# Kernel tuning notes

Hardware: AMD Instinct MI355X
Metric: run time of the kernel (lower is better)

The kernel has to match this reference:

```python
import jax, jax.numpy as jnp
import numpy as np

K = 7          # involution kernel size
PAD = 3        # (K-1)//2
G = 4          # groups = out_channels // group_channels
GC = 16        # group_channels
EPS = 1e-5     # BatchNorm eps


def _bn(x, g, b, m, v):
    # eval-mode BatchNorm2d over channel dim of NCHW
    scale = g / jnp.sqrt(v + EPS)
    return x * scale[:, None, None] + (b - m * scale)[:, None, None]


def _conv1x1(x, w, b=None):
    y = jnp.einsum('bchw,oc->bohw', x, w)
    if b is not None:
        y = y + b[:, None, None]
    return y


def _gelu(x):
    return jax.nn.gelu(x, approximate=False)  # torch nn.GELU default (erf)


def _involution(x, wr, gr, br, mr, vr, ws, bs):
    # kernel-generation branch: 1x1 reduce -> BN -> ReLU -> 1x1 span
    r = jax.nn.relu(_bn(_conv1x1(x, wr), gr, br, mr, vr))
    w = _conv1x1(r, ws, bs)                       # [B, G*K*K, H, W]
    B, _, H, W = w.shape
    w = w.reshape(B, G, K * K, H, W)
    # unfold x into KxK patches (channel-major then row-major kernel pos, matching nn.Unfold)
    xp = jnp.pad(x, ((0, 0), (0, 0), (PAD, PAD), (PAD, PAD)))
    patches = jnp.stack([xp[:, :, i:i + H, j:j + W]
                         for i in range(K) for j in range(K)], axis=2)  # [B, C, KK, H, W]
    patches = patches.reshape(B, G, GC, K * K, H, W)
    out = jnp.einsum('bgkhw,bgckhw->bgchw', w, patches)  # per-pixel dynamic kernel apply
    return out.reshape(B, G * GC, H, W)


def setup_inputs() -> dict:
    key = jax.random.key(0)
    ks = jax.random.split(key, 24)
    B, Cin, Cout, H, W = 4, 32, 64, 128, 128
    red = Cout // 4
    n = lambda k, s, sc: jax.random.normal(k, s, jnp.float32) * sc
    u = lambda k, s: jax.random.uniform(k, s, jnp.float32, 0.5, 1.5)
    inp = {
        'x': n(ks[0], (B, Cin, H, W), 1.0),
        'w1': n(ks[1], (Cout, Cin), 0.15),
        # involution: reduce conv + BN, span conv
        'wr': n(ks[2], (red, Cout), 0.12), 'gr': u(ks[3], (red,)), 'br': n(ks[4], (red,), 0.05),
        'mr': n(ks[5], (red,), 0.05), 'vr': u(ks[6], (red,)),
        'ws': n(ks[7], (K * K * G, red), 0.1), 'bs': n(ks[8], (K * K * G,), 0.02),
        # BN after involution
        'g1': u(ks[9], (Cout,)), 'b1': n(ks[10], (Cout,), 0.05),
        'm1': n(ks[11], (Cout,), 0.05), 'v1': u(ks[12], (Cout,)),
        # convblock2
        'w2': n(ks[13], (Cout, Cout), 0.12),
        'g2': u(ks[14], (Cout,)), 'b2': n(ks[15], (Cout,), 0.05),
        'm2': n(ks[16], (Cout,), 0.05), 'v2': u(ks[17], (Cout,)),
        # mapping (residual projection) conv has bias=True by default
        'wm': n(ks[18], (Cout, Cin), 0.15), 'bmap': n(ks[19], (Cout,), 0.02),
        'gm': u(ks[20], (Cout,)), 'betam': n(ks[21], (Cout,), 0.05),
        'mm': n(ks[22], (Cout,), 0.05), 'vm': u(ks[23], (Cout,)),
    }
    return inp


def reference(x, w1, wr, gr, br, mr, vr, ws, bs, g1, b1, m1, v1,
              w2, g2, b2, m2, v2, wm, bmap, gm, betam, mm, vm):
    x1 = _gelu(_conv1x1(x, w1))                                  # convblock
    x1 = _gelu(_bn(_involution(x1, wr, gr, br, mr, vr, ws, bs),
                   g1, b1, m1, v1))                              # involution + BN + GELU
    x1 = _bn(_conv1x1(x1, w2), g2, b2, m2, v2)                   # convblock2
    skip = _bn(_conv1x1(x, wm, bmap), gm, betam, mm, vm)         # mapping (Cin != Cout)
    return _gelu(x1 + skip)
```

## Files before the change

### kernel.cpp

```cpp
#include <hip/hip_runtime.h>
#include <hip/hip_bf16.h>
#include <math.h>

#define HW    16384
#define Bsz   4
#define CIN   32
#define COUT  64
#define RED   16
#define KKN   49
#define GG    4
#define PW    134
#define PPLANE (PW*PW)
#define N16PAD 574592

typedef __hip_bfloat16 bf16;
typedef __attribute__((ext_vector_type(8))) short bf16x8;
typedef __attribute__((ext_vector_type(4))) float f32x4;

__device__ __forceinline__ float gelu_f(float x) {
    return 0.5f * x * (1.0f + erff(x * 0.70710678118654752f));
}
__device__ __forceinline__ void unpack_bf2(unsigned u, float& lo, float& hi) {
    lo = __uint_as_float(u << 16);
    hi = __uint_as_float(u & 0xffff0000u);
}
__device__ __forceinline__ unsigned pack_bf2(float lo, float hi) {
    unsigned a = __float_as_uint(lo), b = __float_as_uint(hi);
    a += 0x7fff + ((a >> 16) & 1);
    b += 0x7fff + ((b >> 16) & 1);
    return (a >> 16) | (b & 0xffff0000u);
}
__device__ __forceinline__ unsigned short bf16r(float v) {
    unsigned a = __float_as_uint(v);
    a += 0x7fff + ((a >> 16) & 1);
    return (unsigned short)(a >> 16);
}

#define OFF_RBUF  9437184
#define OFF_X2B   13631488
#define OFF_PAR   22020096
#define OFF_XBF   22085632
#define PW1T 0
#define PWRT 2048
#define PRSH 3072
#define PSHC (PRSH+16)
#define PSMV (PSHC+64)
#define PSC1 (PSMV+64)
#define PSH1 (PSC1+64)
#define PCAT_F 12288

__global__ __launch_bounds__(256) void k0_init(
    const float* __restrict__ w1, const float* __restrict__ wr,
    const float* __restrict__ gr, const float* __restrict__ br,
    const float* __restrict__ mr, const float* __restrict__ vr,
    const float* __restrict__ g1, const float* __restrict__ b1,
    const float* __restrict__ m1, const float* __restrict__ v1,
    const float* __restrict__ w2, const float* __restrict__ g2,
    const float* __restrict__ b2, const float* __restrict__ m2,
    const float* __restrict__ v2,
    const float* __restrict__ wm, const float* __restrict__ bmap,
    const float* __restrict__ gm, const float* __restrict__ betam,
    const float* __restrict__ mm, const float* __restrict__ vm,
    float* __restrict__ par, uint4* __restrict__ x1pad)
{
    if (blockIdx.x != 0) {
        int i = (blockIdx.x - 1) * 256 + threadIdx.x;
        if (i < N16PAD) x1pad[i] = make_uint4(0u, 0u, 0u, 0u);
        return;
    }
    int t = threadIdx.x;
    for (int i = t; i < 2048; i += 256) {
        int c = i >> 6, o = i & 63;
        par[PW1T + i] = w1[o * CIN + c];
    }
    for (int i = t; i < 1024; i += 256) {
        int c = i >> 4, j = i & 15;
        float sc = gr[j] * rsqrtf(vr[j] + 1e-5f);
        par[PWRT + i] = wr[j * COUT + c] * sc;
    }
    unsigned short* wcat = (unsigned short*)(par + PCAT_F);
    for (int i = t; i < 64 * 96; i += 256) {
        int o = i / 96, c = i - o * 96;
        float v;
        if (c < 64) {
            float s2 = g2[o] * rsqrtf(v2[o] + 1e-5f);
            float sm = gm[o] * rsqrtf(vm[o] + 1e-5f);
            v = w2[o * COUT + c] * (s2 / sm);
        } else {
            v = wm[o * CIN + (c - 64)];
        }
        wcat[i] = bf16r(v);
    }
    if (t < 16) {
        float sc = gr[t] * rsqrtf(vr[t] + 1e-5f);
        par[PRSH + t] = br[t] - mr[t] * sc;
    }
    if (t < 64) {
        float s2 = g2[t] * rsqrtf(v2[t] + 1e-5f);
        float sm = gm[t] * rsqrtf(vm[t] + 1e-5f);
        par[PSHC + t] = (b2[t] - m2[t] * s2) + (betam[t] + (bmap[t] - mm[t]) * sm);
        par[PSMV + t] = sm;
        float s1 = g1[t] * rsqrtf(v1[t] + 1e-5f);
        par[PSC1 + t] = s1;
        par[PSH1 + t] = b1[t] - m1[t] * s1;
    }
}

__global__ __launch_bounds__(256, 4) void k1_conv1_gelu_reduce(
    const float* __restrict__ x, const float* __restrict__ par,
    unsigned* __restrict__ x1pad, float* __restrict__ rbuf,
    unsigned short* __restrict__ xbf)
{
    __shared__ float g_lds[COUT][65];

    int lane  = threadIdx.x & 63;
    int chunk = __builtin_amdgcn_readfirstlane(threadIdx.x >> 6);
    int b     = blockIdx.x >> 8;
    int p     = ((blockIdx.x & 255) << 6) + lane;
    int h = p >> 7, w = p & 127;

    float xv[CIN];
#pragma unroll
    for (int c = 0; c < CIN; ++c) xv[c] = x[(b * CIN + c) * HW + p];

    if (chunk == 0) {
        unsigned pkx[16];
#pragma unroll
        for (int d = 0; d < 16; ++d) pkx[d] = pack_bf2(xv[2 * d], xv[2 * d + 1]);
        unsigned* xo2 = (unsigned*)&xbf[((size_t)(b * HW + p)) * 32];
        *(uint4*)xo2        = make_uint4(pkx[0], pkx[1], pkx[2], pkx[3]);
        *(uint4*)(xo2 + 4)  = make_uint4(pkx[4], pkx[5], pkx[6], pkx[7]);
        *(uint4*)(xo2 + 8)  = make_uint4(pkx[8], pkx[9], pkx[10], pkx[11]);
        *(uint4*)(xo2 + 12) = make_uint4(pkx[12], pkx[13], pkx[14], pkx[15]);
    }

    float acc[16];
#pragma unroll
    for (int o = 0; o < 16; ++o) acc[o] = 0.f;
#pragma unroll 8
    for (int c = 0; c < CIN; ++c) {
        float xc = xv[c];
        const float* wrow = par + PW1T + c * 64 + chunk * 16;
#pragma unroll
        for (int o = 0; o < 16; ++o) acc[o] += xc * wrow[o];
    }

    unsigned pk[8];
#pragma unroll
    for (int o = 0; o < 16; ++o) {
        acc[o] = gelu_f(acc[o]);
        g_lds[chunk * 16 + o][lane] = acc[o];
    }
#pragma unroll
    for (int d = 0; d < 8; ++d) pk[d] = pack_bf2(acc[2 * d], acc[2 * d + 1]);
    unsigned* xo = x1pad + ((size_t)((b * GG + chunk) * PW + (h + 3)) * PW + (w + 3)) * 8;
    *(uint4*)xo       = make_uint4(pk[0], pk[1], pk[2], pk[3]);
    *(uint4*)(xo + 4) = make_uint4(pk[4], pk[5], pk[6], pk[7]);

    __syncthreads();

    float ra[4] = {0.f, 0.f, 0.f, 0.f};
#pragma unroll 8
    for (int c = 0; c < COUT; ++c) {
        float gv = g_lds[c][lane];
        const float* wrow = par + PWRT + c * 16 + chunk * 4;
#pragma unroll
        for (int jj = 0; jj < 4; ++jj) ra[jj] += gv * wrow[jj];
    }
    float t[4];
#pragma unroll
    for (int jj = 0; jj < 4; ++jj)
        t[jj] = fmaxf(ra[jj] + par[PRSH + chunk * 4 + jj], 0.f);
    *(float4*)&rbuf[((size_t)b * HW + p) * 16 + chunk * 4] =
        make_float4(t[0], t[1], t[2], t[3]);
}

__global__ __launch_bounds__(256, 4) void k23_involution(
    const unsigned* __restrict__ x1pad, const float* __restrict__ rbuf,
    const float* __restrict__ wsp, const float* __restrict__ bsp,
    const float* __restrict__ par, unsigned* __restrict__ x2b)
{
    int bg = blockIdx.x >> 6;
    int g = bg & 3, b = bg >> 2;
    int p = ((blockIdx.x & 63) << 8) + threadIdx.x;
    int h = p >> 7, w0 = p & 127;

    float r[RED];
    {
        const float4* rp = (const float4*)&rbuf[((size_t)b * HW + p) * 16];
        float4 r0 = rp[0], r1 = rp[1], r2 = rp[2], r3 = rp[3];
        r[0]=r0.x; r[1]=r0.y; r[2]=r0.z; r[3]=r0.w;
        r[4]=r1.x; r[5]=r1.y; r[6]=r1.z; r[7]=r1.w;
        r[8]=r2.x; r[9]=r2.y; r[10]=r2.z; r[11]=r2.w;
        r[12]=r3.x; r[13]=r3.y; r[14]=r3.z; r[15]=r3.w;
    }

    const float* wrow = wsp + g * KKN * RED;
    const float* brow = bsp + g * KKN;
    const unsigned* base = x1pad + ((size_t)(bg * PW + h) * PW + w0) * 8;

    float acc[RED];
#pragma unroll
    for (int c = 0; c < RED; ++c) acc[c] = 0.f;

#pragma unroll 1
    for (int i = 0; i < 7; ++i) {
#pragma unroll 1
        for (int j = 0; j < 7; ++j) {
            int k = i * 7 + j;
            const float* wk_row = wrow + k * RED;
            float s = brow[k];
#pragma unroll
            for (int jj = 0; jj < RED; ++jj) s += r[jj] * wk_row[jj];
            const unsigned* tp = base + (size_t)(i * PW + j) * 8;
            uint4 A = *(const uint4*)tp;
            uint4 B = *(const uint4*)(tp + 4);
            float lo, hi;
            unpack_bf2(A.x, lo, hi); acc[0] += s*lo; acc[1] += s*hi;
            unpack_bf2(A.y, lo, hi); acc[2] += s*lo; acc[3] += s*hi;
            unpack_bf2(A.z, lo, hi); acc[4] += s*lo; acc[5] += s*hi;
            unpack_bf2(A.w, lo, hi); acc[6] += s*lo; acc[7] += s*hi;
            unpack_bf2(B.x, lo, hi); acc[8] += s*lo; acc[9] += s*hi;
            unpack_bf2(B.y, lo, hi); acc[10]+= s*lo; acc[11]+= s*hi;
            unpack_bf2(B.z, lo, hi); acc[12]+= s*lo; acc[13]+= s*hi;
            unpack_bf2(B.w, lo, hi); acc[14]+= s*lo; acc[15]+= s*hi;
        }
    }

    unsigned pk[8];
#pragma unroll
    for (int d = 0; d < 8; ++d) {
        int ch0 = g * RED + 2 * d, ch1 = ch0 + 1;
        float v0 = gelu_f(par[PSC1 + ch0] * acc[2 * d]     + par[PSH1 + ch0]);
        float v1 = gelu_f(par[PSC1 + ch1] * acc[2 * d + 1] + par[PSH1 + ch1]);
        pk[d] = pack_bf2(v0, v1);
    }
    unsigned* xo = x2b + ((size_t)bg * HW + p) * 8;
    *(uint4*)xo       = make_uint4(pk[0], pk[1], pk[2], pk[3]);
    *(uint4*)(xo + 4) = make_uint4(pk[4], pk[5], pk[6], pk[7]);
}

__global__ __launch_bounds__(256, 4) void k4_mfma(
    const unsigned short* __restrict__ x2s, const unsigned short* __restrict__ xbf,
    const float* __restrict__ par, float* __restrict__ out)
{
    int lane = threadIdx.x & 63;
    int wave = threadIdx.x >> 6;
    int m15  = lane & 15;
    int quad = lane >> 4;
    int b    = blockIdx.x >> 8;
    int px0  = (((blockIdx.x & 255) << 2) + wave) << 4;

    const unsigned short* wcat = (const unsigned short*)(par + PCAT_F);

    bf16x8 Bf[3][4];
#pragma unroll
    for (int kt = 0; kt < 3; ++kt)
#pragma unroll
        for (int nt = 0; nt < 4; ++nt)
            Bf[kt][nt] = *(const bf16x8*)&wcat[(nt * 16 + m15) * 96 + kt * 32 + quad * 8];

    int px = px0 + m15;
    bf16x8 Af[3];
    {
        int g0 = quad >> 1, co = (quad & 1) * 8;
        Af[0] = *(const bf16x8*)&x2s[((size_t)((b * 4 + g0) * HW + px)) * 16 + co];
        Af[1] = *(const bf16x8*)&x2s[((size_t)((b * 4 + 2 + g0) * HW + px)) * 16 + co];
        Af[2] = *(const bf16x8*)&xbf[((size_t)(b * HW + px)) * 32 + quad * 8];
    }

    f32x4 acc[4];
#pragma unroll
    for (int nt = 0; nt < 4; ++nt) acc[nt] = (f32x4){0.f, 0.f, 0.f, 0.f};
#pragma unroll
    for (int kt = 0; kt < 3; ++kt)
#pragma unroll
        for (int nt = 0; nt < 4; ++nt)
            acc[nt] = __builtin_amdgcn_mfma_f32_16x16x32_bf16(
                Af[kt], Bf[kt][nt], acc[nt], 0, 0, 0);

#pragma unroll
    for (int nt = 0; nt < 4; ++nt) {
        int o = nt * 16 + m15;
        float smv = par[PSMV + o], sh = par[PSHC + o];
        float* op = out + (size_t)(b * COUT + o) * HW + px0 + quad * 4;
#pragma unroll
        for (int reg = 0; reg < 4; ++reg)
            op[reg] = gelu_f(smv * acc[nt][reg] + sh);
    }
}

extern "C" void kernel_launch(void* const* d_in, const int* in_sizes, int n_in,
                              void* d_out, int out_size, void* d_ws, size_t ws_size,
                              hipStream_t stream) {
    const float* x    = (const float*)d_in[0];
    const float* w1   = (const float*)d_in[1];
    const float* wr   = (const float*)d_in[2];
    const float* gr   = (const float*)d_in[3];
    const float* br   = (const float*)d_in[4];
    const float* mr   = (const float*)d_in[5];
    const float* vr   = (const float*)d_in[6];
    const float* wsp  = (const float*)d_in[7];
    const float* bsp  = (const float*)d_in[8];
    const float* g1   = (const float*)d_in[9];
    const float* b1   = (const float*)d_in[10];
    const float* m1   = (const float*)d_in[11];
    const float* v1   = (const float*)d_in[12];
    const float* w2   = (const float*)d_in[13];
    const float* g2   = (const float*)d_in[14];
    const float* b2   = (const float*)d_in[15];
    const float* m2   = (const float*)d_in[16];
    const float* v2   = (const float*)d_in[17];
    const float* wm   = (const float*)d_in[18];
    const float* bmap = (const float*)d_in[19];
    const float* gm   = (const float*)d_in[20];
    const float* betam= (const float*)d_in[21];
    const float* mm   = (const float*)d_in[22];
    const float* vm   = (const float*)d_in[23];

    unsigned*       x1pad = (unsigned*)d_ws;
    float*          rbuf  = (float*)((char*)d_ws + OFF_RBUF);
    unsigned*       x2b   = (unsigned*)((char*)d_ws + OFF_X2B);
    float*          par   = (float*)((char*)d_ws + OFF_PAR);
    unsigned short* xbf   = (unsigned short*)((char*)d_ws + OFF_XBF);

    int nzb = (N16PAD + 255) / 256;
    k0_init<<<nzb + 1, 256, 0, stream>>>(w1, wr, gr, br, mr, vr, g1, b1, m1, v1,
                                         w2, g2, b2, m2, v2, wm, bmap, gm, betam,
                                         mm, vm, par, (uint4*)x1pad);
    k1_conv1_gelu_reduce<<<Bsz * HW / 64, 256, 0, stream>>>(x, par, x1pad, rbuf, xbf);
    k23_involution<<<Bsz * GG * HW / 256, 256, 0, stream>>>(
        x1pad, rbuf, wsp, bsp, par, x2b);
    k4_mfma<<<Bsz * HW / 64, 256, 0, stream>>>(
        (const unsigned short*)x2b, xbf, par, (float*)d_out);
}
```

Before: 173.2 us.

## Compute conv1 and reduce conv with bf16 MFMA; move x bf16 packing to init kernel

The first stage (1x1 conv Cin→Cout with GELU, then the reduce 1x1 conv with ReLU) now runs as bf16 MFMA 16x16x32 tiles instead of scalar FMA loops, with weights pre-converted to bf16 in the init kernel. The fp32-to-bf16 packing of x moves into extra blocks of the init kernel, and the new k1 reads that packed bf16 x. GELU outputs are staged in LDS to repack into the padded grouped layout and to feed the reduce MFMA. This trades fp32 precision in the reduce path for bf16 and adds an extra read of xbf.

Measured after the change: 170.5 us. Within noise of the previous version (-1.5%).

```diff
diff --git a/kernel.cpp b/kernel.cpp
--- a/kernel.cpp
+++ b/kernel.cpp
@@ -40,16 +40,17 @@
 #define OFF_X2B   13631488
 #define OFF_PAR   22020096
 #define OFF_XBF   22085632
-#define PW1T 0
-#define PWRT 2048
-#define PRSH 3072
-#define PSHC (PRSH+16)
-#define PSMV (PSHC+64)
-#define PSC1 (PSMV+64)
-#define PSH1 (PSC1+64)
-#define PCAT_F 12288
+#define PRSH_F 0
+#define PSHC_F 16
+#define PSMV_F 80
+#define PSC1_F 144
+#define PSH1_F 208
+#define BW1B 4096
+#define BWRB 8192
+#define BCAT 12288
 
 __global__ __launch_bounds__(256) void k0_init(
+    const float* __restrict__ x,
     const float* __restrict__ w1, const float* __restrict__ wr,
     const float* __restrict__ gr, const float* __restrict__ br,
     const float* __restrict__ mr, const float* __restrict__ vr,
@@ -61,24 +62,42 @@
     const float* __restrict__ wm, const float* __restrict__ bmap,
     const float* __restrict__ gm, const float* __restrict__ betam,
     const float* __restrict__ mm, const float* __restrict__ vm,
-    float* __restrict__ par, uint4* __restrict__ x1pad)
+    char* __restrict__ parb, uint4* __restrict__ x1pad,
+    unsigned short* __restrict__ xbf, int nzb)
 {
-    if (blockIdx.x != 0) {
-        int i = (blockIdx.x - 1) * 256 + threadIdx.x;
+    int bid = blockIdx.x, t = threadIdx.x;
+    if (bid >= 1 && bid <= nzb) {
+        int i = (bid - 1) * 256 + t;
         if (i < N16PAD) x1pad[i] = make_uint4(0u, 0u, 0u, 0u);
         return;
     }
-    int t = threadIdx.x;
-    for (int i = t; i < 2048; i += 256) {
-        int c = i >> 6, o = i & 63;
-        par[PW1T + i] = w1[o * CIN + c];
-    }
-    for (int i = t; i < 1024; i += 256) {
-        int c = i >> 4, j = i & 15;
+    if (bid > nzb) {
+        int gpx = (bid - nzb - 1) * 256 + t;
+        int b = gpx >> 14, p = gpx & (HW - 1);
+        float xv[CIN];
+#pragma unroll
+        for (int c = 0; c < CIN; ++c) xv[c] = x[(b * CIN + c) * HW + p];
+        unsigned pk[16];
+#pragma unroll
+        for (int d = 0; d < 16; ++d) pk[d] = pack_bf2(xv[2 * d], xv[2 * d + 1]);
+        unsigned* xo = (unsigned*)&xbf[(size_t)gpx * 32];
+        *(uint4*)xo        = make_uint4(pk[0], pk[1], pk[2], pk[3]);
+        *(uint4*)(xo + 4)  = make_uint4(pk[4], pk[5], pk[6], pk[7]);
+        *(uint4*)(xo + 8)  = make_uint4(pk[8], pk[9], pk[10], pk[11]);
+        *(uint4*)(xo + 12) = make_uint4(pk[12], pk[13], pk[14], pk[15]);
+        return;
+    }
+    float* parf = (float*)parb;
+    unsigned short* w1b  = (unsigned short*)(parb + BW1B);
+    unsigned short* wrb  = (unsigned short*)(parb + BWRB);
+    unsigned short* wcat = (unsigned short*)(parb + BCAT);
+    for (int i = t; i < 64 * 32; i += 256)
+        w1b[i] = bf16r(w1[i]);
+    for (int i = t; i < 16 * 64; i += 256) {
+        int j = i >> 6;
         float sc = gr[j] * rsqrtf(vr[j] + 1e-5f);
-        par[PWRT + i] = wr[j * COUT + c] * sc;
-    }
-    unsigned short* wcat = (unsigned short*)(par + PCAT_F);
+        wrb[i] = bf16r(wr[i] * sc);
+    }
     for (int i = t; i < 64 * 96; i += 256) {
         int o = i / 96, c = i - o * 96;
         float v;
@@ -93,86 +112,82 @@
     }
     if (t < 16) {
         float sc = gr[t] * rsqrtf(vr[t] + 1e-5f);
-        par[PRSH + t] = br[t] - mr[t] * sc;
+        parf[PRSH_F + t] = br[t] - mr[t] * sc;
     }
     if (t < 64) {
         float s2 = g2[t] * rsqrtf(v2[t] + 1e-5f);
         float sm = gm[t] * rsqrtf(vm[t] + 1e-5f);
-        par[PSHC + t] = (b2[t] - m2[t] * s2) + (betam[t] + (bmap[t] - mm[t]) * sm);
-        par[PSMV + t] = sm;
+        parf[PSHC_F + t] = (b2[t] - m2[t] * s2) + (betam[t] + (bmap[t] - mm[t]) * sm);
+        parf[PSMV_F + t] = sm;
         float s1 = g1[t] * rsqrtf(v1[t] + 1e-5f);
-        par[PSC1 + t] = s1;
-        par[PSH1 + t] = b1[t] - m1[t] * s1;
-    }
-}
-
-__global__ __launch_bounds__(256, 4) void k1_conv1_gelu_reduce(
-    const float* __restrict__ x, const float* __restrict__ par,
-    unsigned* __restrict__ x1pad, float* __restrict__ rbuf,
-    unsigned short* __restrict__ xbf)
+        parf[PSC1_F + t] = s1;
+        parf[PSH1_F + t] = b1[t] - m1[t] * s1;
+    }
+}
+
+__global__ __launch_bounds__(256, 4) void k1_mfma(
+    const unsigned short* __restrict__ xbf, const char* __restrict__ parb,
+    unsigned* __restrict__ x1pad, float* __restrict__ rbuf)
 {
-    __shared__ float g_lds[COUT][65];
-
-    int lane  = threadIdx.x & 63;
-    int chunk = __builtin_amdgcn_readfirstlane(threadIdx.x >> 6);
-    int b     = blockIdx.x >> 8;
-    int p     = ((blockIdx.x & 255) << 6) + lane;
-    int h = p >> 7, w = p & 127;
-
-    float xv[CIN];
-#pragma unroll
-    for (int c = 0; c < CIN; ++c) xv[c] = x[(b * CIN + c) * HW + p];
-
-    if (chunk == 0) {
-        unsigned pkx[16];
-#pragma unroll
-        for (int d = 0; d < 16; ++d) pkx[d] = pack_bf2(xv[2 * d], xv[2 * d + 1]);
-        unsigned* xo2 = (unsigned*)&xbf[((size_t)(b * HW + p)) * 32];
-        *(uint4*)xo2        = make_uint4(pkx[0], pkx[1], pkx[2], pkx[3]);
-        *(uint4*)(xo2 + 4)  = make_uint4(pkx[4], pkx[5], pkx[6], pkx[7]);
-        *(uint4*)(xo2 + 8)  = make_uint4(pkx[8], pkx[9], pkx[10], pkx[11]);
-        *(uint4*)(xo2 + 12) = make_uint4(pkx[12], pkx[13], pkx[14], pkx[15]);
-    }
-
-    float acc[16];
-#pragma unroll
-    for (int o = 0; o < 16; ++o) acc[o] = 0.f;
-#pragma unroll 8
-    for (int c = 0; c < CIN; ++c) {
-        float xc = xv[c];
-        const float* wrow = par + PW1T + c * 64 + chunk * 16;
-#pragma unroll
-        for (int o = 0; o < 16; ++o) acc[o] += xc * wrow[o];
-    }
-
-    unsigned pk[8];
-#pragma unroll
-    for (int o = 0; o < 16; ++o) {
-        acc[o] = gelu_f(acc[o]);
-        g_lds[chunk * 16 + o][lane] = acc[o];
-    }
-#pragma unroll
-    for (int d = 0; d < 8; ++d) pk[d] = pack_bf2(acc[2 * d], acc[2 * d + 1]);
-    unsigned* xo = x1pad + ((size_t)((b * GG + chunk) * PW + (h + 3)) * PW + (w + 3)) * 8;
-    *(uint4*)xo       = make_uint4(pk[0], pk[1], pk[2], pk[3]);
-    *(uint4*)(xo + 4) = make_uint4(pk[4], pk[5], pk[6], pk[7]);
+    __shared__ float x1f[4][16][65];
+
+    int lane = threadIdx.x & 63;
+    int wave = threadIdx.x >> 6;
+    int m15 = lane & 15, quad = lane >> 4;
+    int base_gpx = blockIdx.x * 64 + wave * 16;
+    int b   = base_gpx >> 14;
+    int px0 = base_gpx & (HW - 1);
+
+    const unsigned short* w1b = (const unsigned short*)(parb + BW1B);
+    const unsigned short* wrb = (const unsigned short*)(parb + BWRB);
+    const float* parf = (const float*)parb;
+
+    bf16x8 Af = *(const bf16x8*)&xbf[((size_t)(base_gpx + m15)) * 32 + quad * 8];
+    f32x4 acc[4];
+#pragma unroll
+    for (int nt = 0; nt < 4; ++nt) {
+        bf16x8 Bf = *(const bf16x8*)&w1b[(nt * 16 + m15) * 32 + quad * 8];
+        f32x4 z = {0.f, 0.f, 0.f, 0.f};
+        acc[nt] = __builtin_amdgcn_mfma_f32_16x16x32_bf16(Af, Bf, z, 0, 0, 0);
+    }
+#pragma unroll
+    for (int nt = 0; nt < 4; ++nt)
+#pragma unroll
+        for (int reg = 0; reg < 4; ++reg)
+            x1f[wave][quad * 4 + reg][nt * 16 + m15] = gelu_f(acc[nt][reg]);
 
     __syncthreads();
 
-    float ra[4] = {0.f, 0.f, 0.f, 0.f};
-#pragma unroll 8
-    for (int c = 0; c < COUT; ++c) {
-        float gv = g_lds[c][lane];
-        const float* wrow = par + PWRT + c * 16 + chunk * 4;
-#pragma unroll
-        for (int jj = 0; jj < 4; ++jj) ra[jj] += gv * wrow[jj];
-    }
-    float t[4];
-#pragma unroll
-    for (int jj = 0; jj < 4; ++jj)
-        t[jj] = fmaxf(ra[jj] + par[PRSH + chunk * 4 + jj], 0.f);
-    *(float4*)&rbuf[((size_t)b * HW + p) * 16 + chunk * 4] =
-        make_float4(t[0], t[1], t[2], t[3]);
+    {
+        int pxl = lane >> 2, g = lane & 3;
+        int p = px0 + pxl, h = p >> 7, w = p & 127;
+        unsigned pk[8];
+#pragma unroll
+        for (int d = 0; d < 8; ++d)
+            pk[d] = pack_bf2(x1f[wave][pxl][g * 16 + 2 * d],
+                             x1f[wave][pxl][g * 16 + 2 * d + 1]);
+        unsigned* xo = x1pad +
+            ((size_t)((b * GG + g) * PW + (h + 3)) * PW + (w + 3)) * 8;
+        *(uint4*)xo       = make_uint4(pk[0], pk[1], pk[2], pk[3]);
+        *(uint4*)(xo + 4) = make_uint4(pk[4], pk[5], pk[6], pk[7]);
+    }
+
+    f32x4 racc = {0.f, 0.f, 0.f, 0.f};
+#pragma unroll
+    for (int kt = 0; kt < 2; ++kt) {
+        bf16x8 A2, B2;
+#pragma unroll
+        for (int j = 0; j < 8; ++j)
+            A2[j] = (short)bf16r(x1f[wave][m15][kt * 32 + quad * 8 + j]);
+        B2 = *(const bf16x8*)&wrb[m15 * 64 + kt * 32 + quad * 8];
+        racc = __builtin_amdgcn_mfma_f32_16x16x32_bf16(A2, B2, racc, 0, 0, 0);
+    }
+    float rsh = parf[PRSH_F + m15];
+#pragma unroll
+    for (int reg = 0; reg < 4; ++reg) {
+        int gp = base_gpx + quad * 4 + reg;
+        rbuf[(size_t)gp * 16 + m15] = fmaxf(racc[reg] + rsh, 0.f);
+    }
 }
 
 __global__ __launch_bounds__(256, 4) void k23_involution(
@@ -231,8 +246,8 @@
 #pragma unroll
     for (int d = 0; d < 8; ++d) {
         int ch0 = g * RED + 2 * d, ch1 = ch0 + 1;
-        float v0 = gelu_f(par[PSC1 + ch0] * acc[2 * d]     + par[PSH1 + ch0]);
-        float v1 = gelu_f(par[PSC1 + ch1] * acc[2 * d + 1] + par[PSH1 + ch1]);
+        float v0 = gelu_f(par[PSC1_F + ch0] * acc[2 * d]     + par[PSH1_F + ch0]);
+        float v1 = gelu_f(par[PSC1_F + ch1] * acc[2 * d + 1] + par[PSH1_F + ch1]);
         pk[d] = pack_bf2(v0, v1);
     }
     unsigned* xo = x2b + ((size_t)bg * HW + p) * 8;
@@ -242,7 +257,7 @@
 
 __global__ __launch_bounds__(256, 4) void k4_mfma(
     const unsigned short* __restrict__ x2s, const unsigned short* __restrict__ xbf,
-    const float* __restrict__ par, float* __restrict__ out)
+    const char* __restrict__ parb, float* __restrict__ out)
 {
     int lane = threadIdx.x & 63;
     int wave = threadIdx.x >> 6;
@@ -251,7 +266,8 @@
     int b    = blockIdx.x >> 8;
     int px0  = (((blockIdx.x & 255) << 2) + wave) << 4;
 
-    const unsigned short* wcat = (const unsigned short*)(par + PCAT_F);
+    const unsigned short* wcat = (const unsigned short*)(parb + BCAT);
+    const float* parf = (const float*)parb;
 
     bf16x8 Bf[3][4];
 #pragma unroll
@@ -282,7 +298,7 @@
 #pragma unroll
     for (int nt = 0; nt < 4; ++nt) {
         int o = nt * 16 + m15;
-        float smv = par[PSMV + o], sh = par[PSHC + o];
+        float smv = parf[PSMV_F + o], sh = parf[PSHC_F + o];
         float* op = out + (size_t)(b * COUT + o) * HW + px0 + quad * 4;
 #pragma unroll
         for (int reg = 0; reg < 4; ++reg)
@@ -321,16 +337,18 @@
     unsigned*       x1pad = (unsigned*)d_ws;
     float*          rbuf  = (float*)((char*)d_ws + OFF_RBUF);
     unsigned*       x2b   = (unsigned*)((char*)d_ws + OFF_X2B);
-    float*          par   = (float*)((char*)d_ws + OFF_PAR);
+    char*           parb  = (char*)d_ws + OFF_PAR;
     unsigned short* xbf   = (unsigned short*)((char*)d_ws + OFF_XBF);
 
     int nzb = (N16PAD + 255) / 256;
-    k0_init<<<nzb + 1, 256, 0, stream>>>(w1, wr, gr, br, mr, vr, g1, b1, m1, v1,
-                                         w2, g2, b2, m2, v2, wm, bmap, gm, betam,
-                                         mm, vm, par, (uint4*)x1pad);
-    k1_conv1_gelu_reduce<<<Bsz * HW / 64, 256, 0, stream>>>(x, par, x1pad, rbuf, xbf);
+    int nxb = Bsz * HW / 256;
+    k0_init<<<1 + nzb + nxb, 256, 0, stream>>>(
+        x, w1, wr, gr, br, mr, vr, g1, b1, m1, v1,
+        w2, g2, b2, m2, v2, wm, bmap, gm, betam, mm, vm,
+        parb, (uint4*)x1pad, xbf, nzb);
+    k1_mfma<<<Bsz * HW / 64, 256, 0, stream>>>(xbf, parb, x1pad, rbuf);
     k23_involution<<<Bsz * GG * HW / 256, 256, 0, stream>>>(
-        x1pad, rbuf, wsp, bsp, par, x2b);
+        x1pad, rbuf, wsp, bsp, (const float*)parb, x2b);
     k4_mfma<<<Bsz * HW / 64, 256, 0, stream>>>(
-        (const unsigned short*)x2b, xbf, par, (float*)d_out);
-}
+        (const unsigned short*)x2b, xbf, parb, (float*)d_out);
+}
```
